# Optimization experiments

Measured on AMD Instinct MI355X. Metric: run time of the kernel, lower is better.

The kernel has to match this reference:

```python
import jax, jax.numpy as jnp
import numpy as np

B, N = 8, 4096  # batch of epidemic trajectories, nodes in the contact network


def setup_inputs() -> dict:
    key = jax.random.key(0)
    k1, k2, k3, k4 = jax.random.split(key, 4)
    state = jax.random.uniform(k1, (B, 4, N), dtype=jnp.float32)
    state = state / state.sum(axis=1, keepdims=True)  # per-node SEIR distribution
    ISNet = jax.random.uniform(k2, (N, N), dtype=jnp.float32)  # dense contact weights in [0,1)
    # small transition probs so rows sum < 1 (expand_psMatrix stays a valid stochastic matrix)
    psMatrix = jax.random.uniform(k3, (4, 4), dtype=jnp.float32) * 0.05
    U = jax.random.uniform(k4, (N,), dtype=jnp.float32)  # torch.rand(n) draw, shared across batch
    return {"state": state, "ISNet": ISNet, "psMatrix": psMatrix, "U": U}


def _expand_ps(psMatrix):
    # eye * (1 - row_sum) + psMatrix  (adds the stay-in-state probability)
    stable = 1.0 - psMatrix.sum(axis=1)
    return jnp.eye(4, dtype=psMatrix.dtype) * stable + psMatrix


def _step(state, ISNet, psMatrix):
    psM = _expand_ps(psMatrix)
    p01 = psM[0, 1]
    # lp[b,j,k] = log(1 - ISNet[j,k] * S_b[j] * I_b[k] * p01)   (vectorized over batch)
    lp = jnp.log(1.0 - ISNet[None, :, :] * state[:, 0, :, None] * state[:, 2, None, :] * p01)
    ps1 = 1.0 - jnp.exp(lp.sum(axis=2))  # [B, N] infection probability per node
    zeros = jnp.zeros_like(ps1)
    ps10 = jnp.stack([1.0 - ps1, ps1, zeros, zeros], axis=1)  # [B, 4, N]
    # constantM zeroes the S row of psM before the transpose-matmul
    mask = jnp.array([[0.0, 0, 0, 0], [1, 1, 1, 1], [1, 1, 1, 1], [1, 1, 1, 1]], dtype=psM.dtype)
    ps2T = (psM * mask).T  # [4, 4]
    return state[:, 0][:, None, :] * ps10 + jnp.einsum('ij,bjn->bin', ps2T, state)


def _sample(P, U):
    # cumulative-threshold sampling: first compartment whose running sum crosses U fires
    u = jnp.broadcast_to(U[None, :], P[:, 0, :].shape)  # [B, N], shared draw across batch
    outs = []
    for i in range(P.shape[1]):  # fixed 4 compartments
        u = u - P[:, i, :]
        s = (u < 0).astype(P.dtype)
        outs.append(s)
        u = u + s
    return jnp.stack(outs, axis=1)  # [B, 4, N] one-hot per node


def reference(state, ISNet, psMatrix, U):
    new_state = _step(state, ISNet, psMatrix)
    return _sample(new_state, U)
```

## Files before the change

### kernel.cpp

```cpp
#include <hip/hip_runtime.h>

#define NN 4096
#define BB 8
#define JT 4
#define KS 2
#define KH (NN / KS)
#define CK 512
#define NC (KH / CK)


__device__ __forceinline__ float2 pk_mul(float2 a, float2 b) {
    return make_float2(a.x * b.x, a.y * b.y);
}
__device__ __forceinline__ float2 pk_add(float2 a, float2 b) {
    return make_float2(a.x + b.x, a.y + b.y);
}
__device__ __forceinline__ float2 pk_fnma(float2 a, float2 b, float2 c) {
    return make_float2(fmaf(-a.x, b.x, c.x), fmaf(-a.y, b.y, c.y));
}

__global__ __launch_bounds__(256, 5) void epi_partial(
    const float* __restrict__ state,
    const float* __restrict__ ISNet,
    const float* __restrict__ psMatrix,
    double* __restrict__ ws)
{
    const int ks   = blockIdx.x & (KS - 1);
    const int jb   = blockIdx.x >> 1;
    const int j0   = jb * JT;
    const int tid  = threadIdx.x;
    const int wave = tid >> 6;
    const int lane = tid & 63;
    const int j    = j0 + wave;
    const int kb   = ks * KH;

    __shared__ float ilds[2][BB][CK];

    const float p01 = psMatrix[1];

    float  cf[BB];
    double prod[BB];
    #pragma unroll
    for (int b = 0; b < BB; ++b) {
        cf[b]   = state[(size_t)b * 4 * NN + j] * p01;
        prod[b] = 1.0;
    }

    const float4* __restrict__ wrow4 = (const float4*)(ISNet + (size_t)j * NN + kb);

    const int sr = tid >> 5;
    const int sc = tid & 31;
    const float4* __restrict__ isrc =
        (const float4*)(state + ((size_t)sr * 4 + 2) * NN + kb);

    float4 sreg[4];
    float4 wcur[2], wnxt[2];

    #pragma unroll
    for (int q = 0; q < 4; ++q) sreg[q] = isrc[sc + 32 * q];
    #pragma unroll
    for (int g = 0; g < 2; ++g) wcur[g] = wrow4[g * 64 + lane];
    #pragma unroll
    for (int q = 0; q < 4; ++q)
        *((float4*)&ilds[0][sr][(sc + 32 * q) * 4]) = sreg[q];

    for (int c = 0; c < NC; ++c) {
        __syncthreads();

        if (c + 1 < NC) {
            const int base = (c + 1) * (CK / 4);
            #pragma unroll
            for (int q = 0; q < 4; ++q) sreg[q] = isrc[base + sc + 32 * q];
            #pragma unroll
            for (int g = 0; g < 2; ++g) wnxt[g] = wrow4[base + g * 64 + lane];
        }

        #pragma unroll
        for (int it = 0; it < 2; ++it) {
            const float4 wv  = wcur[it];
            const float2 w01 = make_float2(wv.x, wv.y);
            const float2 w23 = make_float2(wv.z, wv.w);
            #pragma unroll
            for (int b = 0; b < BB; ++b) {
                const float4 I = *((const float4*)&ilds[c & 1][b][(it * 64 + lane) * 4]);
                const float2 c2  = make_float2(cf[b], cf[b]);
                const float2 z01 = pk_mul(pk_mul(c2, w01), make_float2(I.x, I.y));
                const float2 z23 = pk_mul(pk_mul(c2, w23), make_float2(I.z, I.w));
                const float2 q2  = pk_fnma(z01, z23, pk_add(z01, z23));
                const float  q   = fmaf(-q2.x, q2.y, q2.x + q2.y);
                prod[b] = fma(-(double)q, prod[b], prod[b]);
            }
        }

        if (c + 1 < NC) {
            #pragma unroll
            for (int q = 0; q < 4; ++q)
                *((float4*)&ilds[(c + 1) & 1][sr][(sc + 32 * q) * 4]) = sreg[q];
            wcur[0] = wnxt[0];
            wcur[1] = wnxt[1];
        }
    }

    #pragma unroll
    for (int off = 32; off >= 8; off >>= 1) {
        #pragma unroll
        for (int b = 0; b < BB; ++b)
            prod[b] *= __shfl_xor(prod[b], off, 64);
    }
    const int g = lane >> 3;
    double v = prod[0];
    #pragma unroll
    for (int b = 1; b < BB; ++b) v = (g == b) ? prod[b] : v;
    v *= __shfl_down(v, 4, 64);
    v *= __shfl_down(v, 2, 64);
    v *= __shfl_down(v, 1, 64);

    if ((lane & 7) == 0)
        ws[((size_t)ks * BB + g) * NN + j] = v;
}

__global__ __launch_bounds__(256) void epi_combine(
    const float* __restrict__ state,
    const float* __restrict__ psMatrix,
    const float* __restrict__ U,
    const double* __restrict__ ws,
    float* __restrict__ out)
{
    const int p = blockIdx.x * 256 + threadIdx.x;
    const int b = p >> 12;
    const int j = p & (NN - 1);

    const double tot = ws[(size_t)b * NN + j] * ws[((size_t)BB * NN) + (size_t)b * NN + j];
    const double ps1 = 1.0 - tot;

    double pm[4][4];
    #pragma unroll
    for (int r = 0; r < 4; ++r) {
        double s = 0.0;
        #pragma unroll
        for (int q = 0; q < 4; ++q) {
            pm[r][q] = (double)psMatrix[r * 4 + q];
            s += pm[r][q];
        }
        pm[r][r] += (1.0 - s);
    }

    double st[4];
    #pragma unroll
    for (int r = 0; r < 4; ++r)
        st[r] = (double)state[(size_t)b * 4 * NN + r * NN + j];

    const double S = st[0];
    const double ps10[4] = {1.0 - ps1, ps1, 0.0, 0.0};

    double P[4];
    #pragma unroll
    for (int i = 0; i < 4; ++i) {
        double acc = S * ps10[i];
        #pragma unroll
        for (int r = 1; r < 4; ++r)
            acc += pm[r][i] * st[r];
        P[i] = acc;
    }

    double u = (double)U[j];
    #pragma unroll
    for (int i = 0; i < 4; ++i) {
        u -= P[i];
        const double s = (u < 0.0) ? 1.0 : 0.0;
        out[(size_t)b * 4 * NN + i * NN + j] = (float)s;
        u += s;
    }
}

__global__ __launch_bounds__(256, 4) void epi_fallback(
    const float* __restrict__ state, const float* __restrict__ ISNet,
    const float* __restrict__ psMatrix, const float* __restrict__ U,
    float* __restrict__ out)
{
    const int j0 = blockIdx.x * JT;
    const int tid = threadIdx.x;
    const int wave = tid >> 6, lane = tid & 63;
    const int b0 = wave * 2;
    const float p01 = psMatrix[1];
    float cf[JT][2]; double prod[JT][2];
    #pragma unroll
    for (int jj = 0; jj < JT; ++jj)
        #pragma unroll
        for (int bi = 0; bi < 2; ++bi) {
            cf[jj][bi] = state[(size_t)(b0 + bi) * 4 * NN + (j0 + jj)] * p01;
            prod[jj][bi] = 1.0;
        }
    const float4* __restrict__ w0 = (const float4*)(ISNet + (size_t)(j0 + 0) * NN);
    const float4* __restrict__ w1 = (const float4*)(ISNet + (size_t)(j0 + 1) * NN);
    const float4* __restrict__ w2 = (const float4*)(ISNet + (size_t)(j0 + 2) * NN);
    const float4* __restrict__ w3 = (const float4*)(ISNet + (size_t)(j0 + 3) * NN);
    const float4* __restrict__ i0 = (const float4*)(state + ((size_t)(b0 + 0) * 4 + 2) * NN);
    const float4* __restrict__ i1 = (const float4*)(state + ((size_t)(b0 + 1) * 4 + 2) * NN);
    float4 wA[JT], wB[JT], wC[JT], ia[2], ib[2];
#define LW(BUF, IDX) do { const int _x = lane + (IDX) * 64; \
        BUF[0] = w0[_x]; BUF[1] = w1[_x]; BUF[2] = w2[_x]; BUF[3] = w3[_x]; } while (0)
#define LI(BUF, IDX) do { const int _x = lane + (IDX) * 64; \
        BUF[0] = i0[_x]; BUF[1] = i1[_x]; } while (0)
    auto compute = [&](const float4 (&W)[JT], const float4 (&I)[2]) {
        #pragma unroll
        for (int jj = 0; jj < JT; ++jj) {
            const float2 w01 = make_float2(W[jj].x, W[jj].y);
            const float2 w23 = make_float2(W[jj].z, W[jj].w);
            #pragma unroll
            for (int bi = 0; bi < 2; ++bi) {
                const float4& I4 = bi ? I[1] : I[0];
                const float2 c2 = make_float2(cf[jj][bi], cf[jj][bi]);
                const float2 z01 = pk_mul(pk_mul(c2, w01), make_float2(I4.x, I4.y));
                const float2 z23 = pk_mul(pk_mul(c2, w23), make_float2(I4.z, I4.w));
                const float2 q2 = pk_fnma(z01, z23, pk_add(z01, z23));
                const float q = fmaf(-q2.x, q2.y, q2.x + q2.y);
                prod[jj][bi] = fma(-(double)q, prod[jj][bi], prod[jj][bi]);
            }
        }
    };
#define STEP(W, I, K) do { compute(W, I); \
        if ((K) + 3 < 16) LW(W, (K) + 3); if ((K) + 2 < 16) LI(I, (K) + 2); } while (0)
    LW(wA, 0); LI(ia, 0); LW(wB, 1); LI(ib, 1); LW(wC, 2);
    STEP(wA, ia, 0);  STEP(wB, ib, 1);  STEP(wC, ia, 2);  STEP(wA, ib, 3);
    STEP(wB, ia, 4);  STEP(wC, ib, 5);  STEP(wA, ia, 6);  STEP(wB, ib, 7);
    STEP(wC, ia, 8);  STEP(wA, ib, 9);  STEP(wB, ia, 10); STEP(wC, ib, 11);
    STEP(wA, ia, 12); STEP(wB, ib, 13); STEP(wC, ia, 14); STEP(wA, ib, 15);
#undef STEP
#undef LW
#undef LI
    #pragma unroll
    for (int off = 32; off >= 8; off >>= 1)
        #pragma unroll
        for (int jj = 0; jj < JT; ++jj)
            #pragma unroll
            for (int bi = 0; bi < 2; ++bi)
                prod[jj][bi] *= __shfl_xor(prod[jj][bi], off, 64);
    const int g = lane >> 3;
    double v = prod[0][0];
    v = (g == 1) ? prod[0][1] : v; v = (g == 2) ? prod[1][0] : v;
    v = (g == 3) ? prod[1][1] : v; v = (g == 4) ? prod[2][0] : v;
    v = (g == 5) ? prod[2][1] : v; v = (g == 6) ? prod[3][0] : v;
    v = (g == 7) ? prod[3][1] : v;
    v *= __shfl_down(v, 4, 64); v *= __shfl_down(v, 2, 64); v *= __shfl_down(v, 1, 64);
    __shared__ double red[JT][BB];
    if ((lane & 7) == 0) red[g >> 1][b0 + (g & 1)] = v;
    __syncthreads();
    if (tid < JT * BB) {
        const int jj = tid >> 3, b = tid & 7;
        const int j = j0 + jj;
        const double ps1 = 1.0 - red[jj][b];
        double pm[4][4];
        #pragma unroll
        for (int r = 0; r < 4; ++r) {
            double s = 0.0;
            #pragma unroll
            for (int q = 0; q < 4; ++q) { pm[r][q] = (double)psMatrix[r * 4 + q]; s += pm[r][q]; }
            pm[r][r] += (1.0 - s);
        }
        double st[4];
        #pragma unroll
        for (int r = 0; r < 4; ++r) st[r] = (double)state[(size_t)b * 4 * NN + r * NN + j];
        const double S = st[0];
        const double ps10[4] = {1.0 - ps1, ps1, 0.0, 0.0};
        double P[4];
        #pragma unroll
        for (int i = 0; i < 4; ++i) {
            double acc = S * ps10[i];
            #pragma unroll
            for (int r = 1; r < 4; ++r) acc += pm[r][i] * st[r];
            P[i] = acc;
        }
        double u = (double)U[j];
        #pragma unroll
        for (int i = 0; i < 4; ++i) {
            u -= P[i];
            const double s = (u < 0.0) ? 1.0 : 0.0;
            out[(size_t)b * 4 * NN + i * NN + j] = (float)s;
            u += s;
        }
    }
}

extern "C" void kernel_launch(void* const* d_in, const int* in_sizes, int n_in,
                              void* d_out, int out_size, void* d_ws, size_t ws_size,
                              hipStream_t stream) {
    const float* state    = (const float*)d_in[0];
    const float* ISNet    = (const float*)d_in[1];
    const float* psMatrix = (const float*)d_in[2];
    const float* U        = (const float*)d_in[3];
    float* out            = (float*)d_out;

    const size_t need = (size_t)KS * BB * NN * sizeof(double);
    if (ws_size >= need) {
        double* ws = (double*)d_ws;
        epi_partial<<<(NN / JT) * KS, 256, 0, stream>>>(state, ISNet, psMatrix, ws);
        epi_combine<<<(BB * NN) / 256, 256, 0, stream>>>(state, psMatrix, U, ws, out);
    } else {
        epi_fallback<<<NN / JT, 256, 0, stream>>>(state, ISNet, psMatrix, U, out);
    }
}
```

Measured before the change: 28.65 us.

## Register-tile 4 rows x 4 batches per wave, drop LDS staging

Replaces the per-wave single-row, all-batch loop that staged infected-state vectors through double-buffered LDS with a register tile of 4 ISNet rows by 4 batches per wave. Each block now covers 4 rows, with its waves split over batch halves and K halves, which halves the grid. All loads go straight from global memory into registers with a two-stage software pipeline. This removes __syncthreads and LDS traffic and reuses each W and I load across 4 products, at the cost of more registers (launch bounds lowered to 4) and redundant global reads of the state vectors that rely on cache.

```diff
diff --git a/kernel.cpp b/kernel.cpp
--- a/kernel.cpp
+++ b/kernel.cpp
@@ -3,10 +3,9 @@
 #define NN 4096
 #define BB 8
 #define JT 4
+#define BT 4
 #define KS 2
 #define KH (NN / KS)
-#define CK 512
-#define NC (KH / CK)
 
 
 __device__ __forceinline__ float2 pk_mul(float2 a, float2 b) {
@@ -19,104 +18,113 @@
     return make_float2(fmaf(-a.x, b.x, c.x), fmaf(-a.y, b.y, c.y));
 }
 
-__global__ __launch_bounds__(256, 5) void epi_partial(
+__global__ __launch_bounds__(256, 4) void epi_partial(
     const float* __restrict__ state,
     const float* __restrict__ ISNet,
     const float* __restrict__ psMatrix,
     double* __restrict__ ws)
 {
-    const int ks   = blockIdx.x & (KS - 1);
-    const int jb   = blockIdx.x >> 1;
-    const int j0   = jb * JT;
+    const int j0   = blockIdx.x * JT;
     const int tid  = threadIdx.x;
     const int wave = tid >> 6;
     const int lane = tid & 63;
-    const int j    = j0 + wave;
+    const int bg   = wave & 1;
+    const int ks   = wave >> 1;
+    const int b0   = bg * BT;
     const int kb   = ks * KH;
 
-    __shared__ float ilds[2][BB][CK];
-
     const float p01 = psMatrix[1];
 
-    float  cf[BB];
-    double prod[BB];
-    #pragma unroll
-    for (int b = 0; b < BB; ++b) {
-        cf[b]   = state[(size_t)b * 4 * NN + j] * p01;
-        prod[b] = 1.0;
-    }
-
-    const float4* __restrict__ wrow4 = (const float4*)(ISNet + (size_t)j * NN + kb);
-
-    const int sr = tid >> 5;
-    const int sc = tid & 31;
-    const float4* __restrict__ isrc =
-        (const float4*)(state + ((size_t)sr * 4 + 2) * NN + kb);
-
-    float4 sreg[4];
-    float4 wcur[2], wnxt[2];
-
-    #pragma unroll
-    for (int q = 0; q < 4; ++q) sreg[q] = isrc[sc + 32 * q];
-    #pragma unroll
-    for (int g = 0; g < 2; ++g) wcur[g] = wrow4[g * 64 + lane];
-    #pragma unroll
-    for (int q = 0; q < 4; ++q)
-        *((float4*)&ilds[0][sr][(sc + 32 * q) * 4]) = sreg[q];
-
-    for (int c = 0; c < NC; ++c) {
-        __syncthreads();
-
-        if (c + 1 < NC) {
-            const int base = (c + 1) * (CK / 4);
-            #pragma unroll
-            for (int q = 0; q < 4; ++q) sreg[q] = isrc[base + sc + 32 * q];
-            #pragma unroll
-            for (int g = 0; g < 2; ++g) wnxt[g] = wrow4[base + g * 64 + lane];
-        }
-
-        #pragma unroll
-        for (int it = 0; it < 2; ++it) {
-            const float4 wv  = wcur[it];
-            const float2 w01 = make_float2(wv.x, wv.y);
-            const float2 w23 = make_float2(wv.z, wv.w);
-            #pragma unroll
-            for (int b = 0; b < BB; ++b) {
-                const float4 I = *((const float4*)&ilds[c & 1][b][(it * 64 + lane) * 4]);
-                const float2 c2  = make_float2(cf[b], cf[b]);
-                const float2 z01 = pk_mul(pk_mul(c2, w01), make_float2(I.x, I.y));
-                const float2 z23 = pk_mul(pk_mul(c2, w23), make_float2(I.z, I.w));
+    float  cf[JT][BT];
+    double prod[JT][BT];
+    #pragma unroll
+    for (int jj = 0; jj < JT; ++jj) {
+        #pragma unroll
+        for (int bi = 0; bi < BT; ++bi) {
+            cf[jj][bi]   = state[(size_t)(b0 + bi) * 4 * NN + (j0 + jj)] * p01;
+            prod[jj][bi] = 1.0;
+        }
+    }
+
+    const float4* __restrict__ w4_0 = (const float4*)(ISNet + (size_t)(j0 + 0) * NN + kb);
+    const float4* __restrict__ w4_1 = (const float4*)(ISNet + (size_t)(j0 + 1) * NN + kb);
+    const float4* __restrict__ w4_2 = (const float4*)(ISNet + (size_t)(j0 + 2) * NN + kb);
+    const float4* __restrict__ w4_3 = (const float4*)(ISNet + (size_t)(j0 + 3) * NN + kb);
+    const float4* __restrict__ i4_0 = (const float4*)(state + ((size_t)(b0 + 0) * 4 + 2) * NN + kb);
+    const float4* __restrict__ i4_1 = (const float4*)(state + ((size_t)(b0 + 1) * 4 + 2) * NN + kb);
+    const float4* __restrict__ i4_2 = (const float4*)(state + ((size_t)(b0 + 2) * 4 + 2) * NN + kb);
+    const float4* __restrict__ i4_3 = (const float4*)(state + ((size_t)(b0 + 3) * 4 + 2) * NN + kb);
+
+    float4 wA[JT], wB[JT], iA[BT], iB[BT];
+
+#define LD(W, I, IT)                                        \
+    do {                                                    \
+        const int _x = lane + (IT) * 64;                    \
+        W[0] = w4_0[_x]; W[1] = w4_1[_x];                   \
+        W[2] = w4_2[_x]; W[3] = w4_3[_x];                   \
+        I[0] = i4_0[_x]; I[1] = i4_1[_x];                   \
+        I[2] = i4_2[_x]; I[3] = i4_3[_x];                   \
+    } while (0)
+
+    auto compute = [&](const float4 (&W)[JT], const float4 (&I)[BT]) {
+        #pragma unroll
+        for (int jj = 0; jj < JT; ++jj) {
+            const float2 w01 = make_float2(W[jj].x, W[jj].y);
+            const float2 w23 = make_float2(W[jj].z, W[jj].w);
+            #pragma unroll
+            for (int bi = 0; bi < BT; ++bi) {
+                const float2 c2  = make_float2(cf[jj][bi], cf[jj][bi]);
+                const float2 z01 = pk_mul(pk_mul(c2, w01), make_float2(I[bi].x, I[bi].y));
+                const float2 z23 = pk_mul(pk_mul(c2, w23), make_float2(I[bi].z, I[bi].w));
                 const float2 q2  = pk_fnma(z01, z23, pk_add(z01, z23));
                 const float  q   = fmaf(-q2.x, q2.y, q2.x + q2.y);
-                prod[b] = fma(-(double)q, prod[b], prod[b]);
+                prod[jj][bi] = fma(-(double)q, prod[jj][bi], prod[jj][bi]);
             }
         }
-
-        if (c + 1 < NC) {
-            #pragma unroll
-            for (int q = 0; q < 4; ++q)
-                *((float4*)&ilds[(c + 1) & 1][sr][(sc + 32 * q) * 4]) = sreg[q];
-            wcur[0] = wnxt[0];
-            wcur[1] = wnxt[1];
-        }
-    }
+    };
+
+#define STEP(W, I, K)                                       \
+    do {                                                    \
+        compute(W, I);                                      \
+        if ((K) + 2 < 8) LD(W, I, (K) + 2);                 \
+    } while (0)
+
+    LD(wA, iA, 0); LD(wB, iB, 1);
+    STEP(wA, iA, 0); STEP(wB, iB, 1); STEP(wA, iA, 2); STEP(wB, iB, 3);
+    STEP(wA, iA, 4); STEP(wB, iB, 5); STEP(wA, iA, 6); STEP(wB, iB, 7);
+#undef STEP
+#undef LD
 
     #pragma unroll
     for (int off = 32; off >= 8; off >>= 1) {
         #pragma unroll
-        for (int b = 0; b < BB; ++b)
-            prod[b] *= __shfl_xor(prod[b], off, 64);
-    }
+        for (int jj = 0; jj < JT; ++jj) {
+            #pragma unroll
+            for (int bi = 0; bi < BT; ++bi)
+                prod[jj][bi] *= __shfl_xor(prod[jj][bi], off, 64);
+        }
+    }
+
     const int g = lane >> 3;
-    double v = prod[0];
-    #pragma unroll
-    for (int b = 1; b < BB; ++b) v = (g == b) ? prod[b] : v;
-    v *= __shfl_down(v, 4, 64);
-    v *= __shfl_down(v, 2, 64);
-    v *= __shfl_down(v, 1, 64);
-
-    if ((lane & 7) == 0)
-        ws[((size_t)ks * BB + g) * NN + j] = v;
+    double v0 = prod[0][0], v1 = prod[0][1];
+    v0 = (g == 1) ? prod[0][2] : v0;  v1 = (g == 1) ? prod[0][3] : v1;
+    v0 = (g == 2) ? prod[1][0] : v0;  v1 = (g == 2) ? prod[1][1] : v1;
+    v0 = (g == 3) ? prod[1][2] : v0;  v1 = (g == 3) ? prod[1][3] : v1;
+    v0 = (g == 4) ? prod[2][0] : v0;  v1 = (g == 4) ? prod[2][1] : v1;
+    v0 = (g == 5) ? prod[2][2] : v0;  v1 = (g == 5) ? prod[2][3] : v1;
+    v0 = (g == 6) ? prod[3][0] : v0;  v1 = (g == 6) ? prod[3][1] : v1;
+    v0 = (g == 7) ? prod[3][2] : v0;  v1 = (g == 7) ? prod[3][3] : v1;
+    v0 *= __shfl_down(v0, 4, 64);  v1 *= __shfl_down(v1, 4, 64);
+    v0 *= __shfl_down(v0, 2, 64);  v1 *= __shfl_down(v1, 2, 64);
+    v0 *= __shfl_down(v0, 1, 64);  v1 *= __shfl_down(v1, 1, 64);
+
+    if ((lane & 7) == 0) {
+        const int jj  = g >> 1;
+        const int bi0 = (g & 1) * 2;
+        const int j   = j0 + jj;
+        ws[((size_t)ks * BB + (b0 + bi0 + 0)) * NN + j] = v0;
+        ws[((size_t)ks * BB + (b0 + bi0 + 1)) * NN + j] = v1;
+    }
 }
 
 __global__ __launch_bounds__(256) void epi_combine(
@@ -294,7 +302,7 @@
     const size_t need = (size_t)KS * BB * NN * sizeof(double);
     if (ws_size >= need) {
         double* ws = (double*)d_ws;
-        epi_partial<<<(NN / JT) * KS, 256, 0, stream>>>(state, ISNet, psMatrix, ws);
+        epi_partial<<<NN / JT, 256, 0, stream>>>(state, ISNet, psMatrix, ws);
         epi_combine<<<(BB * NN) / 256, 256, 0, stream>>>(state, psMatrix, U, ws, out);
     } else {
         epi_fallback<<<NN / JT, 256, 0, stream>>>(state, ISNet, psMatrix, U, out);
```

New measurement: 50.67 us. 76.8% more time.
